# Kernel optimization log

Hardware: AMD Instinct MI355X
Metric: run time of the kernel (lower is better)

Reference implementation:

```python
import jax, jax.numpy as jnp
from jax import lax
import numpy as np

B, N, NPOINT, NSAMPLE, C = 4, 16384, 1024, 32, 64
RADIUS2 = 0.1 ** 2
BIG = 1e10


def fps(xyz, npoint):
    """Furthest point sampling. xyz: (B,N,3) -> idx (B,npoint) int32."""
    b, n, _ = xyz.shape

    def step(carry, _):
        dists, farthest = carry                      # (B,N), (B,)
        centroid = jnp.take_along_axis(xyz, farthest[:, None, None], axis=1)  # (B,1,3)
        d = jnp.sum((xyz - centroid) ** 2, axis=-1)  # (B,N)
        dists = jnp.minimum(dists, d)
        nxt = jnp.argmax(dists, axis=-1).astype(jnp.int32)
        return (dists, nxt), farthest

    init = (jnp.full((b, n), BIG, xyz.dtype), jnp.zeros((b,), jnp.int32))
    _, idx = lax.scan(step, init, None, length=npoint)
    return jnp.transpose(idx)  # (B,npoint)


def ball_query(xyz, new_xyz, r2, nsample):
    """First nsample neighbor indices within radius; pad with first hit."""
    n = xyz.shape[1]
    d2 = jnp.sum((new_xyz[:, :, None, :] - xyz[:, None, :, :]) ** 2, axis=-1)  # (B,NP,N)
    within = d2 < r2
    score = jnp.where(within, jnp.arange(n, dtype=jnp.int32), n)  # index if inside ball else N
    neg_vals, _ = lax.top_k(-score, nsample)   # smallest scores (earliest indices)
    idx = -neg_vals                            # (B,NP,nsample), ascending
    first = idx[..., 0:1]
    return jnp.where(idx < n, idx, first)


def setup_inputs() -> dict:
    key = jax.random.key(0)
    ks = jax.random.split(key, 8)
    xyz = jax.random.uniform(ks[0], (B, N, 3), dtype=jnp.float32)
    features = jax.random.normal(ks[1], (B, N, C), dtype=jnp.float32)
    cin = 3 + C
    def init_w(k, o, i):
        return jax.random.normal(k, (o, i), dtype=jnp.float32) * (1.0 / np.sqrt(i))
    return {
        "xyz": xyz,
        "features": features,
        "w1": init_w(ks[2], 64, cin), "b1": jnp.zeros((64,), jnp.float32),
        "w2": init_w(ks[3], 64, 64),  "b2": jnp.zeros((64,), jnp.float32),
        "w3": init_w(ks[4], 128, 64), "b3": jnp.zeros((128,), jnp.float32),
    }


def reference(xyz, features, w1, b1, w2, b2, w3, b3):
    # --- FPS sampling of centers ---
    fidx = fps(xyz, NPOINT)                                        # (B,NP)
    new_xyz = jnp.take_along_axis(xyz, fidx[..., None], axis=1)    # (B,NP,3)
    # --- ball-query grouping ---
    nidx = ball_query(xyz, new_xyz, RADIUS2, NSAMPLE)              # (B,NP,NS)
    flat = nidx.reshape(B, NPOINT * NSAMPLE)
    g_xyz = jnp.take_along_axis(xyz, flat[..., None], axis=1).reshape(B, NPOINT, NSAMPLE, 3)
    g_xyz = g_xyz - new_xyz[:, :, None, :]                         # center-relative coords
    g_feat = jnp.take_along_axis(features, flat[..., None], axis=1).reshape(B, NPOINT, NSAMPLE, C)
    h = jnp.concatenate([g_xyz, g_feat], axis=-1)                  # (B,NP,NS,3+C)
    # --- shared 1x1-conv MLP + ReLU ---
    h = jax.nn.relu(jnp.einsum('bpsc,oc->bpso', h, w1) + b1)
    h = jax.nn.relu(jnp.einsum('bpsc,oc->bpso', h, w2) + b2)
    h = jax.nn.relu(jnp.einsum('bpsc,oc->bpso', h, w3) + b3)       # (B,NP,NS,128)
    # --- max pool over neighbors ---
    new_features = jnp.transpose(jnp.max(h, axis=2), (0, 2, 1))    # (B,128,NP)
    return new_xyz, new_features
```

## Files before the change

kernel.cpp:

```cpp
#include <hip/hip_runtime.h>
#include <stdint.h>

#define BB 4
#define NN 16384
#define NPOINT 1024
#define NSAMPLE 32
#define CC 64
#define RADIUS2 0.00999999977648258209228515625f
#define BIGF 1.0e10f

#define FT 512
#define NPAIR 16

typedef float f32x2 __attribute__((ext_vector_type(2)));

__global__ __launch_bounds__(256) void repack_w1(const float* __restrict__ w1,
                                                 float* __restrict__ w1p) {
    int t = threadIdx.x;
    for (int i = t; i < 64 * 68; i += 256) {
        int o = i / 68, c = i % 68;
        w1p[i] = (c < 67) ? w1[o * 67 + c] : 0.0f;
    }
}

template <int CTRL>
__device__ __forceinline__ void amax_step(float& v, int& i) {
    int nv = __builtin_amdgcn_update_dpp(__float_as_int(v), __float_as_int(v),
                                         CTRL, 0xf, 0xf, false);
    int ni = __builtin_amdgcn_update_dpp(i, i, CTRL, 0xf, 0xf, false);
    float fv = __int_as_float(nv);
    if (fv > v || (fv == v && ni < i)) { v = fv; i = ni; }
}
__device__ __forceinline__ void wave_amax(float& v, int& i) {
    amax_step<0x111>(v, i);
    amax_step<0x112>(v, i);
    amax_step<0x114>(v, i);
    amax_step<0x118>(v, i);
    amax_step<0x142>(v, i);
    amax_step<0x143>(v, i);
}

__global__ __launch_bounds__(FT, 2)
void fps_kernel(const float* xyz, float* new_xyz) {
    const int b = blockIdx.x;
    const int t = threadIdx.x;
    const int lane = t & 63;
    const int w = t >> 6;

    __shared__ float sx[NN];
    __shared__ float sy[NN];
    __shared__ float st[3 * NPOINT];
    __shared__ float2 svi[2][8];

    const float* xb = xyz + (size_t)b * NN * 3;

    f32x2 px[NPAIR], py[NPAIR], pz[NPAIR], dd[NPAIR];

#pragma unroll
    for (int k = 0; k < NPAIR; ++k) {
        const float* p = xb + (size_t)6 * (k * FT + t);
        f32x2 a = *(const f32x2*)(p + 0);
        f32x2 bq = *(const f32x2*)(p + 2);
        f32x2 c = *(const f32x2*)(p + 4);
        int g = 2 * (k * FT + t);
        px[k].x = a.x;  py[k].x = a.y;  pz[k].x = bq.x;
        px[k].y = bq.y; py[k].y = c.x;  pz[k].y = c.y;
        *(f32x2*)&sx[g] = px[k];
        *(f32x2*)&sy[g] = py[k];
        dd[k].x = BIGF; dd[k].y = BIGF;
    }
#pragma unroll
    for (int k = 0; k < NPAIR; ++k)
        asm("" : "+v"(px[k]), "+v"(py[k]), "+v"(pz[k]));

    float cx = xb[0], cy = xb[1], cz = xb[2];
    __syncthreads();

    for (int i = 0; i < NPOINT; ++i) {
        if (t == 0) {
            st[3 * i + 0] = cx; st[3 * i + 1] = cy; st[3 * i + 2] = cz;
        }
        if (i == NPOINT - 1) break;

        f32x2 c2x; c2x.x = cx; c2x.y = cx;
        f32x2 c2y; c2y.x = cy; c2y.y = cy;
        f32x2 c2z; c2z.x = cz; c2z.y = cz;

        float mxx = -1.0f, mxy = -1.0f;
#pragma unroll
        for (int k = 0; k < NPAIR; ++k) {
            f32x2 dx = px[k] - c2x;
            f32x2 dy = py[k] - c2y;
            f32x2 dz = pz[k] - c2z;
            f32x2 m0 = dx * dx;
            f32x2 m1 = dy * dy;
            f32x2 m2 = dz * dz;
            f32x2 d  = (m0 + m1) + m2;
            dd[k].x = fminf(dd[k].x, d.x);
            dd[k].y = fminf(dd[k].y, d.y);
            mxx = fmaxf(mxx, dd[k].x);
            mxy = fmaxf(mxy, dd[k].y);
        }
        float bv = fmaxf(mxx, mxy);

        int bj = 0;
#pragma unroll
        for (int k = NPAIR - 1; k >= 0; --k) {
            if (dd[k].y == bv) bj = 2 * k + 1;
            if (dd[k].x == bv) bj = 2 * k;
        }
        int bi = (bj >> 1) * (2 * FT) + 2 * t + (bj & 1);

        wave_amax(bv, bi);
        if (lane == 63) svi[i & 1][w] = make_float2(bv, __int_as_float(bi));
        __syncthreads();

        float2 s = svi[i & 1][lane & 7];
        float v2 = s.x;
        int i2 = __float_as_int(s.y);
        amax_step<0x111>(v2, i2);
        amax_step<0x112>(v2, i2);
        amax_step<0x114>(v2, i2);
        int ixs = __builtin_amdgcn_readlane(i2, 63);

        cx = sx[ixs];
        cy = sy[ixs];
        cz = xb[ixs * 3 + 2];
    }

    __syncthreads();
    float* ob = new_xyz + (size_t)b * NPOINT * 3;
    for (int j = t; j < 3 * NPOINT; j += FT) ob[j] = st[j];
}

__global__ __launch_bounds__(256) void ballquery_kernel(const float* __restrict__ xyz,
                                                        const float* __restrict__ new_xyz,
                                                        int* __restrict__ nidx) {
    const int t = threadIdx.x;
    const int lane = t & 63;
    const int w = t >> 6;
    const int cid = blockIdx.x * 4 + w;
    const int b = cid >> 10;

    __shared__ int list[4][NSAMPLE];

    const float* xb = xyz + (size_t)b * NN * 3;
    const float* c = new_xyz + (size_t)cid * 3;
    float cx = c[0], cy = c[1], cz = c[2];

    int cnt = 0;
    for (int base = 0; base < NN && cnt < NSAMPLE; base += 64) {
        int j = base + lane;
        float dx = __fsub_rn(xb[j * 3 + 0], cx);
        float dy = __fsub_rn(xb[j * 3 + 1], cy);
        float dz = __fsub_rn(xb[j * 3 + 2], cz);
        float d2 = __fadd_rn(__fadd_rn(__fmul_rn(dx, dx), __fmul_rn(dy, dy)),
                             __fmul_rn(dz, dz));
        bool hit = d2 < RADIUS2;
        unsigned long long m = __ballot(hit);
        int pre = __popcll(m & ((1ull << lane) - 1ull));
        if (hit) {
            int pos = cnt + pre;
            if (pos < NSAMPLE) list[w][pos] = j;
        }
        cnt += __popcll(m);
    }
    __syncthreads();
    if (lane < NSAMPLE) {
        int first = list[w][0];
        int v = (lane < cnt) ? list[w][lane] : first;
        nidx[(size_t)cid * NSAMPLE + lane] = v;
    }
}

__global__ __launch_bounds__(256, 2) void mlp_kernel(
    const float* __restrict__ xyz, const float* __restrict__ features,
    const float* __restrict__ new_xyz, const int* __restrict__ nidx,
    const float* __restrict__ w1p, const float* __restrict__ b1,
    const float* __restrict__ w2, const float* __restrict__ b2,
    const float* __restrict__ w3, const float* __restrict__ b3,
    float* __restrict__ out) {
    const int gid = blockIdx.x * 256 + threadIdx.x;
    const int s = gid & 31;
    const int pg = gid >> 5;
    const int b = pg >> 10;
    const int p = pg & 1023;

    const int idx = nidx[gid];
    const float* nc = new_xyz + (size_t)pg * 3;
    const float* pt = xyz + ((size_t)b * NN + idx) * 3;
    float gx = pt[0] - nc[0], gy = pt[1] - nc[1], gz = pt[2] - nc[2];

    float fin[64];
    const float4* fp = (const float4*)(features + ((size_t)b * NN + idx) * CC);
#pragma unroll
    for (int j = 0; j < 16; ++j) {
        float4 q = fp[j];
        fin[4 * j] = q.x; fin[4 * j + 1] = q.y;
        fin[4 * j + 2] = q.z; fin[4 * j + 3] = q.w;
    }

    float h1[64];
#pragma unroll
    for (int o = 0; o < 64; ++o) {
        const float4* wr = (const float4*)(w1p + o * 68);
        float acc = b1[o];
        float4 q0 = wr[0];
        acc = fmaf(q0.x, gx, acc);
        acc = fmaf(q0.y, gy, acc);
        acc = fmaf(q0.z, gz, acc);
        acc = fmaf(q0.w, fin[0], acc);
#pragma unroll
        for (int j = 1; j < 17; ++j) {
            float4 q = wr[j];
            int c0 = 4 * j - 3;
            acc = fmaf(q.x, fin[c0], acc);
            acc = fmaf(q.y, fin[c0 + 1], acc);
            acc = fmaf(q.z, fin[c0 + 2], acc);
            if (c0 + 3 < 64) acc = fmaf(q.w, fin[c0 + 3], acc);
        }
        h1[o] = fmaxf(acc, 0.0f);
    }

    float h2[64];
#pragma unroll
    for (int o = 0; o < 64; ++o) {
        const float4* wr = (const float4*)(w2 + o * 64);
        float acc = b2[o];
#pragma unroll
        for (int j = 0; j < 16; ++j) {
            float4 q = wr[j];
            acc = fmaf(q.x, h1[4 * j], acc);
            acc = fmaf(q.y, h1[4 * j + 1], acc);
            acc = fmaf(q.z, h1[4 * j + 2], acc);
            acc = fmaf(q.w, h1[4 * j + 3], acc);
        }
        h2[o] = fmaxf(acc, 0.0f);
    }

    float* ob = out + (size_t)b * 128 * NPOINT + p;
#pragma unroll
    for (int o = 0; o < 128; ++o) {
        const float4* wr = (const float4*)(w3 + o * 64);
        float acc = b3[o];
#pragma unroll
        for (int j = 0; j < 16; ++j) {
            float4 q = wr[j];
            acc = fmaf(q.x, h2[4 * j], acc);
            acc = fmaf(q.y, h2[4 * j + 1], acc);
            acc = fmaf(q.z, h2[4 * j + 2], acc);
            acc = fmaf(q.w, h2[4 * j + 3], acc);
        }
        float r = fmaxf(acc, 0.0f);
#pragma unroll
        for (int off = 1; off < 32; off <<= 1) {
            float orr = __shfl_xor(r, off);
            r = fmaxf(r, orr);
        }
        if (s == 0) ob[(size_t)o * NPOINT] = r;
    }
}

extern "C" void kernel_launch(void* const* d_in, const int* in_sizes, int n_in,
                              void* d_out, int out_size, void* d_ws, size_t ws_size,
                              hipStream_t stream) {
    const float* xyz = (const float*)d_in[0];
    const float* features = (const float*)d_in[1];
    const float* w1 = (const float*)d_in[2];
    const float* b1 = (const float*)d_in[3];
    const float* w2 = (const float*)d_in[4];
    const float* b2 = (const float*)d_in[5];
    const float* w3 = (const float*)d_in[6];
    const float* b3 = (const float*)d_in[7];

    float* out = (float*)d_out;
    float* new_xyz = out;
    float* new_feat = out + BB * NPOINT * 3;

    int* nidx = (int*)d_ws;
    float* w1p = (float*)((char*)d_ws + (size_t)BB * NPOINT * NSAMPLE * sizeof(int));

    hipLaunchKernelGGL(repack_w1, dim3(1), dim3(256), 0, stream, w1, w1p);
    hipLaunchKernelGGL(fps_kernel, dim3(BB), dim3(FT), 0, stream, xyz, new_xyz);
    hipLaunchKernelGGL(ballquery_kernel, dim3(BB * NPOINT / 4), dim3(256), 0, stream,
                       xyz, new_xyz, nidx);
    hipLaunchKernelGGL(mlp_kernel, dim3(BB * NPOINT * NSAMPLE / 256), dim3(256), 0, stream,
                       xyz, features, new_xyz, nidx, w1p, b1, w2, b2, w3, b3, new_feat);
}
```

Baseline: 2.155 ms.

## Fuse FPS, ball query and MLP into one producer-consumer persistent kernel

```diff
diff --git a/kernel.cpp b/kernel.cpp
--- a/kernel.cpp
+++ b/kernel.cpp
@@ -11,16 +11,20 @@
 
 #define FT 512
 #define NPAIR 16
+#define NCONS 128
+#define NGRP 256
 
 typedef float f32x2 __attribute__((ext_vector_type(2)));
 
 __global__ __launch_bounds__(256) void repack_w1(const float* __restrict__ w1,
-                                                 float* __restrict__ w1p) {
+                                                 float* __restrict__ w1p,
+                                                 int* __restrict__ flags) {
     int t = threadIdx.x;
     for (int i = t; i < 64 * 68; i += 256) {
         int o = i / 68, c = i % 68;
         w1p[i] = (c < 67) ? w1[o * 67 + c] : 0.0f;
     }
+    for (int i = t; i < BB * NPOINT; i += 256) flags[i] = 0;
 }
 
 template <int CTRL>
@@ -41,223 +45,240 @@
 }
 
 __global__ __launch_bounds__(FT, 2)
-void fps_kernel(const float* xyz, float* new_xyz) {
-    const int b = blockIdx.x;
+void uber_kernel(const float* xyz, const float* features,
+                 float* new_xyz, float* out,
+                 const float* __restrict__ w1p, const float* __restrict__ b1,
+                 const float* __restrict__ w2, const float* __restrict__ b2,
+                 const float* __restrict__ w3, const float* __restrict__ b3,
+                 int* flags) {
+    __shared__ float sx[NN];
+    __shared__ float sy[NN];
+    __shared__ float2 svi[2][8];
+    __shared__ int slist[16][NSAMPLE];
+
     const int t = threadIdx.x;
     const int lane = t & 63;
-    const int w = t >> 6;
-
-    __shared__ float sx[NN];
-    __shared__ float sy[NN];
-    __shared__ float st[3 * NPOINT];
-    __shared__ float2 svi[2][8];
-
-    const float* xb = xyz + (size_t)b * NN * 3;
-
-    f32x2 px[NPAIR], py[NPAIR], pz[NPAIR], dd[NPAIR];
-
-#pragma unroll
-    for (int k = 0; k < NPAIR; ++k) {
-        const float* p = xb + (size_t)6 * (k * FT + t);
-        f32x2 a = *(const f32x2*)(p + 0);
-        f32x2 bq = *(const f32x2*)(p + 2);
-        f32x2 c = *(const f32x2*)(p + 4);
-        int g = 2 * (k * FT + t);
-        px[k].x = a.x;  py[k].x = a.y;  pz[k].x = bq.x;
-        px[k].y = bq.y; py[k].y = c.x;  pz[k].y = c.y;
-        *(f32x2*)&sx[g] = px[k];
-        *(f32x2*)&sy[g] = py[k];
-        dd[k].x = BIGF; dd[k].y = BIGF;
+
+    if (blockIdx.x < BB) {
+        const int b = blockIdx.x;
+        const int w = t >> 6;
+        const float* xb = xyz + (size_t)b * NN * 3;
+
+        f32x2 px[NPAIR], py[NPAIR], pz[NPAIR], dd[NPAIR];
+
+#pragma unroll
+        for (int k = 0; k < NPAIR; ++k) {
+            const float* p = xb + (size_t)6 * (k * FT + t);
+            f32x2 a = *(const f32x2*)(p + 0);
+            f32x2 bq = *(const f32x2*)(p + 2);
+            f32x2 c = *(const f32x2*)(p + 4);
+            int g = 2 * (k * FT + t);
+            px[k].x = a.x;  py[k].x = a.y;  pz[k].x = bq.x;
+            px[k].y = bq.y; py[k].y = c.x;  pz[k].y = c.y;
+            *(f32x2*)&sx[g] = px[k];
+            *(f32x2*)&sy[g] = py[k];
+            dd[k].x = BIGF; dd[k].y = BIGF;
+        }
+#pragma unroll
+        for (int k = 0; k < NPAIR; ++k)
+            asm("" : "+v"(px[k]), "+v"(py[k]), "+v"(pz[k]));
+
+        float cx = xb[0], cy = xb[1], cz = xb[2];
+        __syncthreads();
+
+        for (int i = 0; i < NPOINT; ++i) {
+            if (t == 0) {
+                float* o = new_xyz + ((size_t)b * NPOINT + i) * 3;
+                o[0] = cx; o[1] = cy; o[2] = cz;
+                __hip_atomic_store(&flags[b * NPOINT + i], 1,
+                                   __ATOMIC_RELEASE, __HIP_MEMORY_SCOPE_AGENT);
+            }
+            if (i == NPOINT - 1) break;
+
+            f32x2 c2x; c2x.x = cx; c2x.y = cx;
+            f32x2 c2y; c2y.x = cy; c2y.y = cy;
+            f32x2 c2z; c2z.x = cz; c2z.y = cz;
+
+            float mxx = -1.0f, mxy = -1.0f;
+#pragma unroll
+            for (int k = 0; k < NPAIR; ++k) {
+                f32x2 dx = px[k] - c2x;
+                f32x2 dy = py[k] - c2y;
+                f32x2 dz = pz[k] - c2z;
+                f32x2 m0 = dx * dx;
+                f32x2 m1 = dy * dy;
+                f32x2 m2 = dz * dz;
+                f32x2 d  = (m0 + m1) + m2;
+                dd[k].x = fminf(dd[k].x, d.x);
+                dd[k].y = fminf(dd[k].y, d.y);
+                mxx = fmaxf(mxx, dd[k].x);
+                mxy = fmaxf(mxy, dd[k].y);
+            }
+            float bv = fmaxf(mxx, mxy);
+
+            int bj = 0;
+#pragma unroll
+            for (int k = NPAIR - 1; k >= 0; --k) {
+                if (dd[k].y == bv) bj = 2 * k + 1;
+                if (dd[k].x == bv) bj = 2 * k;
+            }
+            int bi = (bj >> 1) * (2 * FT) + 2 * t + (bj & 1);
+
+            wave_amax(bv, bi);
+            if (lane == 63) svi[i & 1][w] = make_float2(bv, __int_as_float(bi));
+            __syncthreads();
+
+            float2 s = svi[i & 1][lane & 7];
+            float v2 = s.x;
+            int i2 = __float_as_int(s.y);
+            amax_step<0x111>(v2, i2);
+            amax_step<0x112>(v2, i2);
+            amax_step<0x114>(v2, i2);
+            int ixs = __builtin_amdgcn_readlane(i2, 63);
+
+            cx = sx[ixs];
+            cy = sy[ixs];
+            cz = xb[ixs * 3 + 2];
+        }
+        return;
     }
-#pragma unroll
-    for (int k = 0; k < NPAIR; ++k)
-        asm("" : "+v"(px[k]), "+v"(py[k]), "+v"(pz[k]));
-
-    float cx = xb[0], cy = xb[1], cz = xb[2];
-    __syncthreads();
-
-    for (int i = 0; i < NPOINT; ++i) {
+
+    const int c = blockIdx.x - BB;
+    int gA = c, gB = (NGRP - 1) - c;
+    if ((gA & 63) > (gB & 63)) { int tq = gA; gA = gB; gB = tq; }
+
+    for (int r = 0; r < 2; ++r) {
+        const int g = (r == 0) ? gA : gB;
+        const int base = g * 16;
+
         if (t == 0) {
-            st[3 * i + 0] = cx; st[3 * i + 1] = cy; st[3 * i + 2] = cz;
-        }
-        if (i == NPOINT - 1) break;
-
-        f32x2 c2x; c2x.x = cx; c2x.y = cx;
-        f32x2 c2y; c2y.x = cy; c2y.y = cy;
-        f32x2 c2z; c2z.x = cz; c2z.y = cz;
-
-        float mxx = -1.0f, mxy = -1.0f;
-#pragma unroll
-        for (int k = 0; k < NPAIR; ++k) {
-            f32x2 dx = px[k] - c2x;
-            f32x2 dy = py[k] - c2y;
-            f32x2 dz = pz[k] - c2z;
-            f32x2 m0 = dx * dx;
-            f32x2 m1 = dy * dy;
-            f32x2 m2 = dz * dz;
-            f32x2 d  = (m0 + m1) + m2;
-            dd[k].x = fminf(dd[k].x, d.x);
-            dd[k].y = fminf(dd[k].y, d.y);
-            mxx = fmaxf(mxx, dd[k].x);
-            mxy = fmaxf(mxy, dd[k].y);
-        }
-        float bv = fmaxf(mxx, mxy);
-
-        int bj = 0;
-#pragma unroll
-        for (int k = NPAIR - 1; k >= 0; --k) {
-            if (dd[k].y == bv) bj = 2 * k + 1;
-            if (dd[k].x == bv) bj = 2 * k;
-        }
-        int bi = (bj >> 1) * (2 * FT) + 2 * t + (bj & 1);
-
-        wave_amax(bv, bi);
-        if (lane == 63) svi[i & 1][w] = make_float2(bv, __int_as_float(bi));
+            int guard = 0;
+            while (__hip_atomic_load(&flags[base + 15], __ATOMIC_ACQUIRE,
+                                     __HIP_MEMORY_SCOPE_AGENT) == 0) {
+                if (++guard > (1 << 18)) break;
+                __builtin_amdgcn_s_sleep(2);
+            }
+        }
         __syncthreads();
 
-        float2 s = svi[i & 1][lane & 7];
-        float v2 = s.x;
-        int i2 = __float_as_int(s.y);
-        amax_step<0x111>(v2, i2);
-        amax_step<0x112>(v2, i2);
-        amax_step<0x114>(v2, i2);
-        int ixs = __builtin_amdgcn_readlane(i2, 63);
-
-        cx = sx[ixs];
-        cy = sy[ixs];
-        cz = xb[ixs * 3 + 2];
-    }
-
-    __syncthreads();
-    float* ob = new_xyz + (size_t)b * NPOINT * 3;
-    for (int j = t; j < 3 * NPOINT; j += FT) ob[j] = st[j];
-}
-
-__global__ __launch_bounds__(256) void ballquery_kernel(const float* __restrict__ xyz,
-                                                        const float* __restrict__ new_xyz,
-                                                        int* __restrict__ nidx) {
-    const int t = threadIdx.x;
-    const int lane = t & 63;
-    const int w = t >> 6;
-    const int cid = blockIdx.x * 4 + w;
-    const int b = cid >> 10;
-
-    __shared__ int list[4][NSAMPLE];
-
-    const float* xb = xyz + (size_t)b * NN * 3;
-    const float* c = new_xyz + (size_t)cid * 3;
-    float cx = c[0], cy = c[1], cz = c[2];
-
-    int cnt = 0;
-    for (int base = 0; base < NN && cnt < NSAMPLE; base += 64) {
-        int j = base + lane;
-        float dx = __fsub_rn(xb[j * 3 + 0], cx);
-        float dy = __fsub_rn(xb[j * 3 + 1], cy);
-        float dz = __fsub_rn(xb[j * 3 + 2], cz);
-        float d2 = __fadd_rn(__fadd_rn(__fmul_rn(dx, dx), __fmul_rn(dy, dy)),
-                             __fmul_rn(dz, dz));
-        bool hit = d2 < RADIUS2;
-        unsigned long long m = __ballot(hit);
-        int pre = __popcll(m & ((1ull << lane) - 1ull));
-        if (hit) {
-            int pos = cnt + pre;
-            if (pos < NSAMPLE) list[w][pos] = j;
-        }
-        cnt += __popcll(m);
-    }
-    __syncthreads();
-    if (lane < NSAMPLE) {
-        int first = list[w][0];
-        int v = (lane < cnt) ? list[w][lane] : first;
-        nidx[(size_t)cid * NSAMPLE + lane] = v;
-    }
-}
-
-__global__ __launch_bounds__(256, 2) void mlp_kernel(
-    const float* __restrict__ xyz, const float* __restrict__ features,
-    const float* __restrict__ new_xyz, const int* __restrict__ nidx,
-    const float* __restrict__ w1p, const float* __restrict__ b1,
-    const float* __restrict__ w2, const float* __restrict__ b2,
-    const float* __restrict__ w3, const float* __restrict__ b3,
-    float* __restrict__ out) {
-    const int gid = blockIdx.x * 256 + threadIdx.x;
-    const int s = gid & 31;
-    const int pg = gid >> 5;
-    const int b = pg >> 10;
-    const int p = pg & 1023;
-
-    const int idx = nidx[gid];
-    const float* nc = new_xyz + (size_t)pg * 3;
-    const float* pt = xyz + ((size_t)b * NN + idx) * 3;
-    float gx = pt[0] - nc[0], gy = pt[1] - nc[1], gz = pt[2] - nc[2];
-
-    float fin[64];
-    const float4* fp = (const float4*)(features + ((size_t)b * NN + idx) * CC);
-#pragma unroll
-    for (int j = 0; j < 16; ++j) {
-        float4 q = fp[j];
-        fin[4 * j] = q.x; fin[4 * j + 1] = q.y;
-        fin[4 * j + 2] = q.z; fin[4 * j + 3] = q.w;
-    }
-
-    float h1[64];
-#pragma unroll
-    for (int o = 0; o < 64; ++o) {
-        const float4* wr = (const float4*)(w1p + o * 68);
-        float acc = b1[o];
-        float4 q0 = wr[0];
-        acc = fmaf(q0.x, gx, acc);
-        acc = fmaf(q0.y, gy, acc);
-        acc = fmaf(q0.z, gz, acc);
-        acc = fmaf(q0.w, fin[0], acc);
-#pragma unroll
-        for (int j = 1; j < 17; ++j) {
-            float4 q = wr[j];
-            int c0 = 4 * j - 3;
-            acc = fmaf(q.x, fin[c0], acc);
-            acc = fmaf(q.y, fin[c0 + 1], acc);
-            acc = fmaf(q.z, fin[c0 + 2], acc);
-            if (c0 + 3 < 64) acc = fmaf(q.w, fin[c0 + 3], acc);
-        }
-        h1[o] = fmaxf(acc, 0.0f);
-    }
-
-    float h2[64];
-#pragma unroll
-    for (int o = 0; o < 64; ++o) {
-        const float4* wr = (const float4*)(w2 + o * 64);
-        float acc = b2[o];
-#pragma unroll
-        for (int j = 0; j < 16; ++j) {
-            float4 q = wr[j];
-            acc = fmaf(q.x, h1[4 * j], acc);
-            acc = fmaf(q.y, h1[4 * j + 1], acc);
-            acc = fmaf(q.z, h1[4 * j + 2], acc);
-            acc = fmaf(q.w, h1[4 * j + 3], acc);
-        }
-        h2[o] = fmaxf(acc, 0.0f);
-    }
-
-    float* ob = out + (size_t)b * 128 * NPOINT + p;
-#pragma unroll
-    for (int o = 0; o < 128; ++o) {
-        const float4* wr = (const float4*)(w3 + o * 64);
-        float acc = b3[o];
-#pragma unroll
-        for (int j = 0; j < 16; ++j) {
-            float4 q = wr[j];
-            acc = fmaf(q.x, h2[4 * j], acc);
-            acc = fmaf(q.y, h2[4 * j + 1], acc);
-            acc = fmaf(q.z, h2[4 * j + 2], acc);
-            acc = fmaf(q.w, h2[4 * j + 3], acc);
-        }
-        float r = fmaxf(acc, 0.0f);
-#pragma unroll
-        for (int off = 1; off < 32; off <<= 1) {
-            float orr = __shfl_xor(r, off);
-            r = fmaxf(r, orr);
-        }
-        if (s == 0) ob[(size_t)o * NPOINT] = r;
+        const int w = t >> 6;
+        for (int q = 0; q < 2; ++q) {
+            const int n = 2 * w + q;
+            const int cid = base + n;
+            const int b_ = cid >> 10;
+            const float* xb = xyz + (size_t)b_ * NN * 3;
+            const float* cc = new_xyz + (size_t)cid * 3;
+            float cx = cc[0], cy = cc[1], cz = cc[2];
+
+            int cnt = 0;
+            for (int bs = 0; bs < NN && cnt < NSAMPLE; bs += 64) {
+                int j = bs + lane;
+                float dx = __fsub_rn(xb[j * 3 + 0], cx);
+                float dy = __fsub_rn(xb[j * 3 + 1], cy);
+                float dz = __fsub_rn(xb[j * 3 + 2], cz);
+                float d2 = __fadd_rn(__fadd_rn(__fmul_rn(dx, dx),
+                                               __fmul_rn(dy, dy)),
+                                     __fmul_rn(dz, dz));
+                bool hit = d2 < RADIUS2;
+                unsigned long long m = __ballot(hit);
+                int pre = __popcll(m & ((1ull << lane) - 1ull));
+                if (hit) {
+                    int pos = cnt + pre;
+                    if (pos < NSAMPLE) slist[n][pos] = j;
+                }
+                cnt += __popcll(m);
+            }
+            if (lane < NSAMPLE) {
+                int first = slist[n][0];
+                int v = (lane < cnt) ? slist[n][lane] : first;
+                slist[n][lane] = v;
+            }
+        }
+        __syncthreads();
+
+        {
+            const int n = t >> 5;
+            const int s = t & 31;
+            const int cid = base + n;
+            const int b_ = cid >> 10;
+            const int p = cid & 1023;
+            const int idx = slist[n][s];
+
+            const float* nc = new_xyz + (size_t)cid * 3;
+            const float* pt = xyz + ((size_t)b_ * NN + idx) * 3;
+            float gx = pt[0] - nc[0], gy = pt[1] - nc[1], gz = pt[2] - nc[2];
+
+            float fin[64];
+            const float4* fp =
+                (const float4*)(features + ((size_t)b_ * NN + idx) * CC);
+#pragma unroll
+            for (int j = 0; j < 16; ++j) {
+                float4 q = fp[j];
+                fin[4 * j] = q.x; fin[4 * j + 1] = q.y;
+                fin[4 * j + 2] = q.z; fin[4 * j + 3] = q.w;
+            }
+
+            float h1[64];
+#pragma unroll
+            for (int o = 0; o < 64; ++o) {
+                const float4* wr = (const float4*)(w1p + o * 68);
+                float acc = b1[o];
+                float4 q0 = wr[0];
+                acc = fmaf(q0.x, gx, acc);
+                acc = fmaf(q0.y, gy, acc);
+                acc = fmaf(q0.z, gz, acc);
+                acc = fmaf(q0.w, fin[0], acc);
+#pragma unroll
+                for (int j = 1; j < 17; ++j) {
+                    float4 q = wr[j];
+                    int c0 = 4 * j - 3;
+                    acc = fmaf(q.x, fin[c0], acc);
+                    acc = fmaf(q.y, fin[c0 + 1], acc);
+                    acc = fmaf(q.z, fin[c0 + 2], acc);
+                    if (c0 + 3 < 64) acc = fmaf(q.w, fin[c0 + 3], acc);
+                }
+                h1[o] = fmaxf(acc, 0.0f);
+            }
+
+            float h2[64];
+#pragma unroll
+            for (int o = 0; o < 64; ++o) {
+                const float4* wr = (const float4*)(w2 + o * 64);
+                float acc = b2[o];
+#pragma unroll
+                for (int j = 0; j < 16; ++j) {
+                    float4 q = wr[j];
+                    acc = fmaf(q.x, h1[4 * j], acc);
+                    acc = fmaf(q.y, h1[4 * j + 1], acc);
+                    acc = fmaf(q.z, h1[4 * j + 2], acc);
+                    acc = fmaf(q.w, h1[4 * j + 3], acc);
+                }
+                h2[o] = fmaxf(acc, 0.0f);
+            }
+
+            float* ob = out + (size_t)b_ * 128 * NPOINT + p;
+#pragma unroll
+            for (int o = 0; o < 128; ++o) {
+                const float4* wr = (const float4*)(w3 + o * 64);
+                float acc = b3[o];
+#pragma unroll
+                for (int j = 0; j < 16; ++j) {
+                    float4 q = wr[j];
+                    acc = fmaf(q.x, h2[4 * j], acc);
+                    acc = fmaf(q.y, h2[4 * j + 1], acc);
+                    acc = fmaf(q.z, h2[4 * j + 2], acc);
+                    acc = fmaf(q.w, h2[4 * j + 3], acc);
+                }
+                float r2 = fmaxf(acc, 0.0f);
+#pragma unroll
+                for (int off = 1; off < 32; off <<= 1) {
+                    float orr = __shfl_xor(r2, off);
+                    r2 = fmaxf(r2, orr);
+                }
+                if (s == 0) ob[(size_t)o * NPOINT] = r2;
+            }
+        }
+        __syncthreads();
     }
 }
 
@@ -277,13 +298,12 @@
     float* new_xyz = out;
     float* new_feat = out + BB * NPOINT * 3;
 
-    int* nidx = (int*)d_ws;
-    float* w1p = (float*)((char*)d_ws + (size_t)BB * NPOINT * NSAMPLE * sizeof(int));
-
-    hipLaunchKernelGGL(repack_w1, dim3(1), dim3(256), 0, stream, w1, w1p);
-    hipLaunchKernelGGL(fps_kernel, dim3(BB), dim3(FT), 0, stream, xyz, new_xyz);
-    hipLaunchKernelGGL(ballquery_kernel, dim3(BB * NPOINT / 4), dim3(256), 0, stream,
-                       xyz, new_xyz, nidx);
-    hipLaunchKernelGGL(mlp_kernel, dim3(BB * NPOINT * NSAMPLE / 256), dim3(256), 0, stream,
-                       xyz, features, new_xyz, nidx, w1p, b1, w2, b2, w3, b3, new_feat);
-}
+    float* w1p = (float*)d_ws;
+    int* flags = (int*)((char*)d_ws + 64 * 68 * sizeof(float));
+
+    hipLaunchKernelGGL(repack_w1, dim3(1), dim3(256), 0, stream, w1, w1p, flags);
+    hipLaunchKernelGGL(uber_kernel, dim3(BB + NCONS), dim3(FT), 0, stream,
+                       xyz, features, new_xyz, out + BB * NPOINT * 3 - 0,
+                       w1p, b1, w2, b2, w3, b3, flags);
+    (void)new_feat;
+}
```

New measurement: 2.809 ms. 1.3x slower.
